# Kernel optimization log

Measured on AMD Instinct MI355X. Metric: run time of the kernel, lower is better.

Reference implementation:

```python
import jax, jax.numpy as jnp
import numpy as np

P, Q, R = 3, 1, 0          # CliffordAlgebra(p=3, q=1, r=0)
N = P + Q + R
ALG = 1 << N               # 16 basis blades
SHIFTS = (1, 2, 4)


def _cayley():
    """Cayley table C[i,j,k]: blade_i * blade_j = C[i,j,i^j] * blade_{i^j}."""
    metric = [1.0] * P + [-1.0] * Q + [0.0] * R
    C = np.zeros((ALG, ALG, ALG), np.float32)
    for a in range(ALG):
        for b in range(ALG):
            x = a >> 1
            s = 0
            while x:                       # reordering sign
                s += bin(x & b).count('1')
                x >>= 1
            val = -1.0 if (s & 1) else 1.0
            for i in range(N):             # metric for repeated basis vectors
                if (a & b) >> i & 1:
                    val *= metric[i]
            C[a, b, a ^ b] = val
    return C

_C = _cayley()
C0 = jnp.asarray(_C[:, :, 0])                        # grade-0 slice: <a*b>_0
A = jnp.asarray((_C - _C.transpose(1, 0, 2)) / 2.0)  # antisym: (ab - ba)/2
VEC_MASK = jnp.asarray(np.array([1.0 if bin(i).count('1') == 1 else 0.0 for i in range(ALG)], np.float32))
BIV_MASK = jnp.asarray(np.array([1.0 if bin(i).count('1') == 2 else 0.0 for i in range(ALG)], np.float32))


def setup_inputs() -> dict:
    key = jax.random.key(0)
    k1, k2 = jax.random.split(key, 2)
    B, T, D = 8, 4096, 1024
    return {
        "x": jax.random.normal(k1, (B, T, D), jnp.float32),
        "gate_w": jax.random.normal(k2, (D, 1), jnp.float32) * 0.02,
        "gate_b": jnp.zeros((1,), jnp.float32),
        "scalar_weight": jnp.float32(0.5),
        "bivector_weight": jnp.float32(0.5),
    }


def reference(x, gate_w, gate_b, scalar_weight, bivector_weight):
    B, T, D = x.shape
    n = D // ALG                         # 64 chunks of 16 (D divisible, no pad)
    ss = jax.nn.sigmoid(scalar_weight)
    sb = jax.nn.sigmoid(bivector_weight)
    gate = jax.nn.sigmoid(x @ gate_w + gate_b)   # (B,T,1), gate of x (loop-invariant)
    xc = x.reshape(B, T, n, ALG)
    out = x
    for shift in SHIFTS:                 # T=4096 > shift always
        c = x - jnp.roll(x, shift, axis=1)
        cc = c.reshape(B, T, n, ALG)
        # inner product: scalar part per chunk, summed over chunks
        scalar = jnp.einsum('btni,btnj,ij->bt', xc, cc, C0)
        # wedge: antisymmetrized geometric product of vector-grade projections
        av = xc * VEC_MASK
        bv = cc * VEC_MASK
        wedge = jnp.einsum('btni,btnj,ijk->btnk', av, bv, A) * BIV_MASK
        delta = (sb * wedge).reshape(B, T, D)
        delta = delta.at[..., 0].add(ss * scalar)   # scalar_part lives at index 0
        out = out + gate * delta
    return out
```

## Files before the change

### kernel.cpp

```cpp
#include <hip/hip_runtime.h>
#include <math.h>


constexpr int T_DIM   = 4096;
constexpr int D_DIM   = 1024;
constexpr int L_STRIP = 16;
constexpr int PF      = 3;
constexpr int WARM    = 4;

constexpr int QB0 = 0x8000;
constexpr int QB1 = 0x8055;
constexpr int QB2 = 0x80AA;

template <int PAT>
__device__ __forceinline__ float swz(float v) {
    return __int_as_float(__builtin_amdgcn_ds_swizzle(__float_as_int(v), PAT));
}

__device__ __forceinline__ float sigmoidf(float z) {
    return 1.0f / (1.0f + __expf(-z));
}

__global__ __launch_bounds__(256, 2) void clifford_kernel(
    const float* __restrict__ x,
    const float* __restrict__ gate_w,
    const float* __restrict__ gate_b,
    const float* __restrict__ scalar_w,
    const float* __restrict__ bivec_w,
    float* __restrict__ out,
    int nstrips)
{
    int blk = blockIdx.x;
    if ((gridDim.x & 7) == 0) {
        const int per = gridDim.x >> 3;
        blk = (blockIdx.x & 7) * per + (blockIdx.x >> 3);
    }

    const int lane  = threadIdx.x & 63;
    const int strip = blk * 4 + (threadIdx.x >> 6);
    if (strip >= nstrips) return;

    const int spb = T_DIM / L_STRIP;
    const int b   = strip / spb;
    const int t0  = (strip - b * spb) * L_STRIP;
    const int sub = lane & 3;
    const int coff = lane << 2;

    const float* __restrict__ xb = x + (size_t)b * T_DIM * D_DIM;
    float*       __restrict__ ob = out + ((size_t)b * T_DIM + t0) * D_DIM;

    float4 s[8][4];
    #pragma unroll
    for (int j = 0; j < WARM + PF; ++j) {
        const int trow = (t0 - WARM + j) & (T_DIM - 1);
        const float* __restrict__ r = xb + (size_t)trow * D_DIM + coff;
        #pragma unroll
        for (int m = 0; m < 4; ++m)
            s[(j + 4) & 7][m] = *(const float4*)(r + (m << 8));
    }
    float4 gv[4];
    #pragma unroll
    for (int m = 0; m < 4; ++m)
        gv[m] = *(const float4*)(gate_w + coff + (m << 8));

    const float ss = sigmoidf(scalar_w[0]);
    const float sb = sigmoidf(bivec_w[0]);
    const float gb = gate_b[0];

    float4 ws;
    if      (sub == 0) ws = make_float4( 1.f,  1.f,  1.f, -1.f);
    else if (sub == 1) ws = make_float4( 1.f, -1.f, -1.f, -1.f);
    else if (sub == 2) ws = make_float4(-1.f,  1.f,  1.f,  1.f);
    else               ws = make_float4( 1.f,  1.f,  1.f, -1.f);
    const float m3  = (sub == 0) ? 1.f : 0.f;
    const float a1  = (sub == 1) ? 1.f : 0.f;
    const float a2  = (sub == 2) ? 1.f : 0.f;
    const float m12 = (sub == 3) ? 1.f : 0.f;

    #pragma unroll
    for (int k = 0; k < L_STRIP; ++k) {
        if (k + PF < L_STRIP) {
            const float* __restrict__ r =
                xb + (size_t)(t0 + k + PF) * D_DIM + coff;
            #pragma unroll
            for (int m = 0; m < 4; ++m)
                s[(k + PF) & 7][m] = *(const float4*)(r + (m << 8));
        }

        float gp = 0.f, sc = 0.f;
        float4 dl[4];

        #pragma unroll
        for (int m = 0; m < 4; ++m) {
            const float4 cur = s[k & 7][m];
            const float4 p1  = s[(k + 7) & 7][m];
            const float4 p2  = s[(k + 6) & 7][m];
            const float4 p4  = s[(k + 4) & 7][m];

            float4 cs;
            cs.x = 3.f * cur.x - p1.x - p2.x - p4.x;
            cs.y = 3.f * cur.y - p1.y - p2.y - p4.y;
            cs.z = 3.f * cur.z - p1.z - p2.z - p4.z;
            cs.w = 3.f * cur.w - p1.w - p2.w - p4.w;

            gp += cur.x * gv[m].x + cur.y * gv[m].y
                + cur.z * gv[m].z + cur.w * gv[m].w;
            sc += ws.x * (cur.x * cs.x) + ws.y * (cur.y * cs.y)
                + ws.z * (cur.z * cs.z) + ws.w * (cur.w * cs.w);

            const float x1  = swz<QB0>(cur.y), x2  = swz<QB0>(cur.z);
            const float x4b = swz<QB1>(cur.x), x8b = swz<QB2>(cur.x);
            const float c1  = swz<QB0>(cs.y),  c2  = swz<QB0>(cs.z);
            const float c4b = swz<QB1>(cs.x),  c8b = swz<QB2>(cs.x);

            const float w3  = x1 * c2  - x2  * c1;
            const float w5  = x1 * c4b - x4b * c1;
            const float w6  = x2 * c4b - x4b * c2;
            const float w9  = x1 * c8b - x8b * c1;
            const float w10 = x2 * c8b - x8b * c2;
            const float w12 = x4b * c8b - x8b * c4b;

            dl[m] = make_float4(m12 * w12,
                                a1 * w5 + a2 * w9,
                                a1 * w6 + a2 * w10,
                                m3 * w3);
        }

        #pragma unroll
        for (int o = 32; o > 0; o >>= 1) {
            gp += __shfl_xor(gp, o, 64);
            sc += __shfl_xor(sc, o, 64);
        }
        const float gate = sigmoidf(gp + gb);
        const float gsb  = gate * sb;

        float* __restrict__ orow = ob + (size_t)k * D_DIM + coff;
        #pragma unroll
        for (int m = 0; m < 4; ++m) {
            const float4 cur = s[k & 7][m];
            float4 o4;
            o4.x = cur.x + gsb * dl[m].x;
            o4.y = cur.y + gsb * dl[m].y;
            o4.z = cur.z + gsb * dl[m].z;
            o4.w = cur.w + gsb * dl[m].w;
            if (m == 0 && lane == 0) o4.x += gate * ss * sc;
            *(float4*)(orow + (m << 8)) = o4;
        }
    }
}

extern "C" void kernel_launch(void* const* d_in, const int* in_sizes, int n_in,
                              void* d_out, int out_size, void* d_ws, size_t ws_size,
                              hipStream_t stream) {
    const float* x  = (const float*)d_in[0];
    const float* gw = (const float*)d_in[1];
    const float* gb = (const float*)d_in[2];
    const float* sw = (const float*)d_in[3];
    const float* bw = (const float*)d_in[4];
    float* out = (float*)d_out;

    const int BT      = in_sizes[0] / D_DIM;
    const int nstrips = BT / L_STRIP;
    const int blocks  = (nstrips + 3) / 4;
    hipLaunchKernelGGL(clifford_kernel, dim3(blocks), dim3(256), 0, stream,
                       x, gw, gb, sw, bw, out, nstrips);
}
```

Baseline: 246.3 us.

## Share time rows across warps via LDS ring buffer instead of per-warp strips

Each block of four warps now processes one contiguous strip of 32 time rows, with warps interleaved by row. Rows are staged in a 16-slot shared-memory ring so each warp reads its shifted neighbours (t-1, t-2, t-4) from LDS instead of each warp reloading four warm-up rows from global memory. This removes the redundant halo reads of the old per-warp strips. In exchange it adds a __syncthreads per iteration, 64KB of LDS per block that limits occupancy, and LDS read traffic.

New measurement: 256.3 us. 1.04x slower.

```diff
diff --git a/kernel.cpp b/kernel.cpp
--- a/kernel.cpp
+++ b/kernel.cpp
@@ -4,9 +4,9 @@
 
 constexpr int T_DIM   = 4096;
 constexpr int D_DIM   = 1024;
-constexpr int L_STRIP = 16;
-constexpr int PF      = 3;
-constexpr int WARM    = 4;
+constexpr int L_STRIP = 32;
+constexpr int NITER   = L_STRIP / 4;
+constexpr int NSLOT   = 16;
 
 constexpr int QB0 = 0x8000;
 constexpr int QB1 = 0x8055;
@@ -28,7 +28,7 @@
     const float* __restrict__ scalar_w,
     const float* __restrict__ bivec_w,
     float* __restrict__ out,
-    int nstrips)
+    int nblocks)
 {
     int blk = blockIdx.x;
     if ((gridDim.x & 7) == 0) {
@@ -36,32 +36,45 @@
         blk = (blockIdx.x & 7) * per + (blockIdx.x >> 3);
     }
 
-    const int lane  = threadIdx.x & 63;
-    const int strip = blk * 4 + (threadIdx.x >> 6);
-    if (strip >= nstrips) return;
+    const int tid  = threadIdx.x;
+    const int wid  = tid >> 6;
+    const int lane = tid & 63;
+    const int sub  = lane & 3;
+    const int coff = lane << 2;
 
     const int spb = T_DIM / L_STRIP;
-    const int b   = strip / spb;
-    const int t0  = (strip - b * spb) * L_STRIP;
-    const int sub = lane & 3;
-    const int coff = lane << 2;
+    const int b   = blk / spb;
+    const int t0  = (blk - b * spb) * L_STRIP;
 
     const float* __restrict__ xb = x + (size_t)b * T_DIM * D_DIM;
-    float*       __restrict__ ob = out + ((size_t)b * T_DIM + t0) * D_DIM;
 
-    float4 s[8][4];
-    #pragma unroll
-    for (int j = 0; j < WARM + PF; ++j) {
-        const int trow = (t0 - WARM + j) & (T_DIM - 1);
-        const float* __restrict__ r = xb + (size_t)trow * D_DIM + coff;
+    __shared__ float ring[NSLOT * D_DIM];
+
+    float4 pa[4], pb[4], st[4], gv[4];
+    {
+        const int ra = (t0 - 4 + wid) & (T_DIM - 1);
+        const int rb = t0 + wid;
+        const float* ga = xb + (size_t)ra * D_DIM + coff;
+        const float* gs = xb + (size_t)rb * D_DIM + coff;
+        #pragma unroll
+        for (int m = 0; m < 4; ++m) {
+            pa[m] = *(const float4*)(ga + (m << 8));
+            pb[m] = *(const float4*)(gs + (m << 8));
+            gv[m] = *(const float4*)(gate_w + coff + (m << 8));
+        }
+        const float* g1 = xb + (size_t)(t0 + 4 + wid) * D_DIM + coff;
         #pragma unroll
         for (int m = 0; m < 4; ++m)
-            s[(j + 4) & 7][m] = *(const float4*)(r + (m << 8));
+            st[m] = *(const float4*)(g1 + (m << 8));
+
+        float* la = &ring[(wid)     * D_DIM] + coff;
+        float* lb = &ring[(wid + 4) * D_DIM] + coff;
+        #pragma unroll
+        for (int m = 0; m < 4; ++m) {
+            *(float4*)(la + (m << 8)) = pa[m];
+            *(float4*)(lb + (m << 8)) = pb[m];
+        }
     }
-    float4 gv[4];
-    #pragma unroll
-    for (int m = 0; m < 4; ++m)
-        gv[m] = *(const float4*)(gate_w + coff + (m << 8));
 
     const float ss = sigmoidf(scalar_w[0]);
     const float sb = sigmoidf(bivec_w[0]);
@@ -77,25 +90,39 @@
     const float a2  = (sub == 2) ? 1.f : 0.f;
     const float m12 = (sub == 3) ? 1.f : 0.f;
 
+    __syncthreads();
+
     #pragma unroll
-    for (int k = 0; k < L_STRIP; ++k) {
-        if (k + PF < L_STRIP) {
-            const float* __restrict__ r =
-                xb + (size_t)(t0 + k + PF) * D_DIM + coff;
+    for (int i = 0; i < NITER; ++i) {
+        if (i + 1 < NITER) {
+            float* l = &ring[((4 * i + 8 + wid) % NSLOT) * D_DIM] + coff;
             #pragma unroll
             for (int m = 0; m < 4; ++m)
-                s[(k + PF) & 7][m] = *(const float4*)(r + (m << 8));
+                *(float4*)(l + (m << 8)) = st[m];
+        }
+        if (i + 2 < NITER) {
+            const float* g = xb + (size_t)(t0 + 4 * i + 8 + wid) * D_DIM + coff;
+            #pragma unroll
+            for (int m = 0; m < 4; ++m)
+                st[m] = *(const float4*)(g + (m << 8));
         }
 
+        const int lq = 4 * i + wid + 4;
+        const float* rc  = &ring[((lq)          % NSLOT) * D_DIM] + coff;
+        const float* rp1 = &ring[((lq - 1)      % NSLOT) * D_DIM] + coff;
+        const float* rp2 = &ring[((lq - 2)      % NSLOT) * D_DIM] + coff;
+        const float* rp4 = &ring[((lq - 4)      % NSLOT) * D_DIM] + coff;
+
         float gp = 0.f, sc = 0.f;
-        float4 dl[4];
+        float4 xv[4], dl[4];
 
         #pragma unroll
         for (int m = 0; m < 4; ++m) {
-            const float4 cur = s[k & 7][m];
-            const float4 p1  = s[(k + 7) & 7][m];
-            const float4 p2  = s[(k + 6) & 7][m];
-            const float4 p4  = s[(k + 4) & 7][m];
+            xv[m] = *(const float4*)(rc + (m << 8));
+            const float4 p1 = *(const float4*)(rp1 + (m << 8));
+            const float4 p2 = *(const float4*)(rp2 + (m << 8));
+            const float4 p4 = *(const float4*)(rp4 + (m << 8));
+            const float4 cur = xv[m];
 
             float4 cs;
             cs.x = 3.f * cur.x - p1.x - p2.x - p4.x;
@@ -134,18 +161,20 @@
         const float gate = sigmoidf(gp + gb);
         const float gsb  = gate * sb;
 
-        float* __restrict__ orow = ob + (size_t)k * D_DIM + coff;
+        const int t = t0 + 4 * i + wid;
+        float* __restrict__ orow = out + ((size_t)b * T_DIM + t) * D_DIM + coff;
         #pragma unroll
         for (int m = 0; m < 4; ++m) {
-            const float4 cur = s[k & 7][m];
             float4 o4;
-            o4.x = cur.x + gsb * dl[m].x;
-            o4.y = cur.y + gsb * dl[m].y;
-            o4.z = cur.z + gsb * dl[m].z;
-            o4.w = cur.w + gsb * dl[m].w;
+            o4.x = xv[m].x + gsb * dl[m].x;
+            o4.y = xv[m].y + gsb * dl[m].y;
+            o4.z = xv[m].z + gsb * dl[m].z;
+            o4.w = xv[m].w + gsb * dl[m].w;
             if (m == 0 && lane == 0) o4.x += gate * ss * sc;
             *(float4*)(orow + (m << 8)) = o4;
         }
+
+        __syncthreads();
     }
 }
 
@@ -160,8 +189,7 @@
     float* out = (float*)d_out;
 
     const int BT      = in_sizes[0] / D_DIM;
-    const int nstrips = BT / L_STRIP;
-    const int blocks  = (nstrips + 3) / 4;
-    hipLaunchKernelGGL(clifford_kernel, dim3(blocks), dim3(256), 0, stream,
-                       x, gw, gb, sw, bw, out, nstrips);
+    const int nblocks = BT / L_STRIP;
+    hipLaunchKernelGGL(clifford_kernel, dim3(nblocks), dim3(256), 0, stream,
+                       x, gw, gb, sw, bw, out, nblocks);
 }
```
